# Optimization experiments

Hardware: AMD Instinct MI355X
Metric: run time of the kernel (lower is better)

Reference implementation:

```python
import jax, jax.numpy as jnp
import numpy as np

B, C, N = 4, 256, 4096
QK = 32  # query/key channel dim hardcoded in module


def setup_inputs() -> dict:
    key = jax.random.key(0)
    ks = jax.random.split(key, 5)
    sc = 1.0 / np.sqrt(C)
    return {
        "x": jax.random.normal(ks[0], (B, C, N), dtype=jnp.float32),
        "Wf": jax.random.normal(ks[1], (QK, C), dtype=jnp.float32) * sc,
        "bf": jnp.zeros((QK,), dtype=jnp.float32),
        "Wg": jax.random.normal(ks[2], (QK, C), dtype=jnp.float32) * sc,
        "bg": jnp.zeros((QK,), dtype=jnp.float32),
        "Wh": jax.random.normal(ks[3], (C, C), dtype=jnp.float32) * sc,
        "bh": jnp.zeros((C,), dtype=jnp.float32),
        "gamma": jax.random.normal(ks[4], (1,), dtype=jnp.float32) * 0.1,
    }


def reference(x, Wf, bf, Wg, bg, Wh, bh, gamma):
    # 1x1 Conv1d == channel-mixing matmul: (O,C) x (B,C,N) -> (B,O,N)
    f = jnp.einsum('oc,bcn->bon', Wf, x) + bf[:, None]   # (B, 32, N)
    g = jnp.einsum('oc,bcn->bon', Wg, x) + bg[:, None]   # (B, 32, N)
    h = jnp.einsum('oc,bcn->bon', Wh, x) + bh[:, None]   # (B, C, N)
    # attention[b, n, m] = sum_k f[b,k,n] * g[b,k,m]  (unscaled, per source)
    attn = jax.nn.softmax(jnp.einsum('bkn,bkm->bnm', f, g), axis=-1)  # (B,N,N)
    # torch.bmm(h, attention): out[b,c,m] = sum_n h[b,c,n] * attn[b,n,m]
    sa = jnp.einsum('bcn,bnm->bcm', h, attn)             # (B, C, N)
    return gamma * sa + x
```

## Files before the change

### kernel.cpp

```cpp
#include <hip/hip_runtime.h>
#include <hip/hip_bf16.h>
#include <math.h>

constexpr int Bb = 4;
constexpr int Cc = 256;
constexpr int Nn = 4096;
constexpr int K  = 32;

constexpr float LOG2E = 1.4426950408889634f;
constexpr float C40L  = 40.0f * LOG2E;

typedef __attribute__((ext_vector_type(8))) short short8;
typedef __attribute__((ext_vector_type(4))) float f32x4;
typedef __attribute__((ext_vector_type(2))) unsigned int uint2v;

static __device__ __forceinline__ unsigned int pack2(float a, float b) {
  union { __hip_bfloat162 h2; unsigned int u; } cv;
  cv.h2 = __float22bfloat162_rn(float2{a, b});
  return cv.u;
}
static __device__ __forceinline__ unsigned short f2bf(float f) {
  union { __hip_bfloat16 h; unsigned short u; } cv;
  cv.h = __float2bfloat16(f);
  return cv.u;
}
static __device__ __forceinline__ f32x4 MF(short8 a, short8 b, f32x4 c) {
  return __builtin_amdgcn_mfma_f32_16x16x32_bf16(a, b, c, 0, 0, 0);
}
static __device__ __forceinline__ float ex2(float v) {
  return __builtin_amdgcn_exp2f(v);
}
static __device__ __forceinline__ void stage16(const unsigned short* g,
                                               unsigned short* l) {
  __builtin_amdgcn_global_load_lds(
      (const __attribute__((address_space(1))) unsigned int*)g,
      (__attribute__((address_space(3))) unsigned int*)l, 16, 0, 0);
}


__global__ __launch_bounds__(256) void castW(
    const float* __restrict__ Wh, unsigned short* __restrict__ Whb)
{
  int i = (blockIdx.x * 256 + threadIdx.x) * 4;
  float4 v = *(const float4*)&Wh[i];
  uint2 o = { pack2(v.x, v.y), pack2(v.z, v.w) };
  *(uint2*)&Whb[i] = o;
}

__global__ __launch_bounds__(256) void castFG(
    const float* __restrict__ Wf, const float* __restrict__ Wg,
    unsigned short* __restrict__ Wfgb)
{
  int g = (blockIdx.x * 256 + threadIdx.x) * 4;
  int row = g >> 8, c = g & 255;
  const float* src = (row < 32) ? &Wf[row*Cc + c] : &Wg[(row-32)*Cc + c];
  float4 v = *(const float4*)src;
  uint2 o = { pack2(v.x, v.y), pack2(v.z, v.w) };
  *(uint2*)&Wfgb[g] = o;
}

__global__ __launch_bounds__(256) void trans_k(
    const float* __restrict__ x, unsigned short* __restrict__ xT)
{
  __shared__ unsigned short Ls[64][65];
  const int b  = blockIdx.z;
  const int n0 = blockIdx.x * 64, c0 = blockIdx.y * 64;
  const int tid = threadIdx.x;
  {
    const int cr = tid >> 4, n4 = (tid & 15) * 4;
#pragma unroll
    for (int rr = 0; rr < 4; ++rr) {
      int c = rr * 16 + cr;
      float4 v = *(const float4*)&x[(size_t)(b*Cc + c0 + c)*Nn + n0 + n4];
      Ls[c][n4+0] = f2bf(v.x); Ls[c][n4+1] = f2bf(v.y);
      Ls[c][n4+2] = f2bf(v.z); Ls[c][n4+3] = f2bf(v.w);
    }
  }
  __syncthreads();
  {
    const int nw = tid >> 4, cw = (tid & 15) * 4;
#pragma unroll
    for (int rr = 0; rr < 4; ++rr) {
      int n = nw + rr * 16;
      unsigned int lo = (unsigned int)Ls[cw+0][n] | ((unsigned int)Ls[cw+1][n] << 16);
      unsigned int hi = (unsigned int)Ls[cw+2][n] | ((unsigned int)Ls[cw+3][n] << 16);
      uint2 o = { lo, hi };
      *(uint2*)&xT[(size_t)(b*Nn + n0 + n)*Cc + c0 + cw] = o;
    }
  }
}

__global__ __launch_bounds__(256) void proj_fgM(
    const unsigned short* __restrict__ xT, const unsigned short* __restrict__ Wfgb,
    const float* __restrict__ bf, const float* __restrict__ bg,
    unsigned short* __restrict__ Ft, unsigned short* __restrict__ Gt)
{
  const int b = blockIdx.y;
  const int tid = threadIdx.x, wave = tid >> 6, lane = tid & 63;
  const int q = lane >> 4, col = lane & 15;
  const int n = blockIdx.x * 64 + wave * 16 + col;

  const unsigned short* Bp = xT + (size_t)(b*Nn + n)*Cc + q*8;
  const f32x4 zero = {0.f,0.f,0.f,0.f};
  f32x4 af0 = zero, af1 = zero, ag0 = zero, ag1 = zero;
#pragma unroll
  for (int kc = 0; kc < 8; ++kc) {
    short8 bn = *(const short8*)(Bp + kc*32);
    short8 a0 = *(const short8*)(Wfgb + (size_t)( 0 + col)*Cc + kc*32 + q*8);
    short8 a1 = *(const short8*)(Wfgb + (size_t)(16 + col)*Cc + kc*32 + q*8);
    short8 a2 = *(const short8*)(Wfgb + (size_t)(32 + col)*Cc + kc*32 + q*8);
    short8 a3 = *(const short8*)(Wfgb + (size_t)(48 + col)*Cc + kc*32 + q*8);
    af0 = MF(a0, bn, af0); af1 = MF(a1, bn, af1);
    ag0 = MF(a2, bn, ag0); ag1 = MF(a3, bn, ag1);
  }
  float4 bf0 = *(const float4*)&bf[q*4],      bf1 = *(const float4*)&bf[16 + q*4];
  float4 bg0 = *(const float4*)&bg[q*4],      bg1 = *(const float4*)&bg[16 + q*4];
  uint2 F0 = { pack2((af0[0]+bf0.x)*LOG2E, (af0[1]+bf0.y)*LOG2E),
               pack2((af0[2]+bf0.z)*LOG2E, (af0[3]+bf0.w)*LOG2E) };
  uint2 F1 = { pack2((af1[0]+bf1.x)*LOG2E, (af1[1]+bf1.y)*LOG2E),
               pack2((af1[2]+bf1.z)*LOG2E, (af1[3]+bf1.w)*LOG2E) };
  uint2 G0 = { pack2(ag0[0]+bg0.x, ag0[1]+bg0.y), pack2(ag0[2]+bg0.z, ag0[3]+bg0.w) };
  uint2 G1 = { pack2(ag1[0]+bg1.x, ag1[1]+bg1.y), pack2(ag1[2]+bg1.z, ag1[3]+bg1.w) };
  unsigned short* fo = Ft + (size_t)(b*Nn + n)*K;
  unsigned short* go = Gt + (size_t)(b*Nn + n)*K;
  *(uint2*)(fo + q*4) = F0;  *(uint2*)(fo + 16 + q*4) = F1;
  *(uint2*)(go + q*4) = G0;  *(uint2*)(go + 16 + q*4) = G1;
}

__global__ __launch_bounds__(512) void pass1(
    const unsigned short* __restrict__ Ft, const unsigned short* __restrict__ Gt,
    unsigned short* __restrict__ Et, float* __restrict__ Lp)
{
  __shared__ float red[8][64];
  const int n0 = blockIdx.x * 64;
  const int mh = blockIdx.y;
  const int b  = blockIdx.z;
  const int tid = threadIdx.x, wave = tid >> 6, lane = tid & 63;
  const int q = lane >> 4, col = lane & 15;
  const unsigned short* Fb = Ft + (size_t)b*Nn*K;
  const unsigned short* Gb = Gt + (size_t)b*Nn*K;
  unsigned short* Ebt = Et + (size_t)b*Nn*Nn;

  short8 af[4];
#pragma unroll
  for (int rb = 0; rb < 4; ++rb)
    af[rb] = *(const short8*)(Fb + (size_t)(n0 + rb*16 + col)*K + q*8);

  const int mw = mh*2048 + wave*256;
  const f32x4 cinit = {-C40L, -C40L, -C40L, -C40L};
  float l[16];
#pragma unroll
  for (int i = 0; i < 16; ++i) l[i] = 0.f;

  unsigned short* sbase = Ebt + (size_t)(n0 >> 3)*128
                        + (q >> 1)*128 + col*8 + (q & 1)*4;

  short8 gA = *(const short8*)(Gb + (size_t)(mw + col)*K + q*8);
  for (int it = 0; it < 16; ++it) {
    short8 gB = *(const short8*)(Gb + (size_t)(mw + ((it+1)&15)*16 + col)*K + q*8);
    f32x4 ts[4];
    ts[0] = MF(af[0], gA, cinit);
    ts[1] = MF(af[1], gA, cinit);
    ts[2] = MF(af[2], gA, cinit);
    ts[3] = MF(af[3], gA, cinit);
    const int mt = (mw >> 4) + it;
    unsigned short* sb = sbase + (size_t)mt * (Nn*16);
#pragma unroll
    for (int rb = 0; rb < 4; ++rb) {
      float e0 = ex2(ts[rb][0]), e1 = ex2(ts[rb][1]);
      float e2 = ex2(ts[rb][2]), e3 = ex2(ts[rb][3]);
      l[rb*4+0] += e0; l[rb*4+1] += e1; l[rb*4+2] += e2; l[rb*4+3] += e3;
      uint2v w = { pack2(e0, e1), pack2(e2, e3) };
      __builtin_nontemporal_store(w, (uint2v*)(sb + rb*256));
    }
    gA = gB;
  }
#pragma unroll
  for (int d = 1; d < 16; d <<= 1) {
#pragma unroll
    for (int i = 0; i < 16; ++i) l[i] += __shfl_xor(l[i], d);
  }
  if (col == 0) {
#pragma unroll
    for (int rb = 0; rb < 4; ++rb) {
      float4 v = {l[rb*4+0], l[rb*4+1], l[rb*4+2], l[rb*4+3]};
      *(float4*)&red[wave][rb*16 + q*4] = v;
    }
  }
  __syncthreads();
  if (tid < 64) {
    float t = 0.f;
#pragma unroll
    for (int w = 0; w < 8; ++w) t += red[w][tid];
    Lp[((size_t)mh*Bb + b)*Nn + n0 + tid] = t;
  }
}

__global__ __launch_bounds__(256) void sumL(
    const float* __restrict__ Lp, float* __restrict__ L)
{
  int i = blockIdx.x * 256 + threadIdx.x;
  L[i] = Lp[i] + Lp[(size_t)Bb*Nn + i];
}

__global__ __launch_bounds__(256) void proj_hT(
    const unsigned short* __restrict__ xT, const unsigned short* __restrict__ Whb,
    const float* __restrict__ bh, const float* __restrict__ L,
    const float* __restrict__ gamma, unsigned short* __restrict__ Ht)
{
  const int b   = blockIdx.z;
  const int n0  = blockIdx.x * 64;
  const int c0  = blockIdx.y * 64;
  const int tid = threadIdx.x;
  const int wave = tid >> 6, lane = tid & 63;
  const int q = lane >> 4, col = lane & 15;
  const int nw = n0 + wave * 16;

  const unsigned short* Arow  = xT  + (size_t)(b*Nn + nw + col) * Cc + q*8;
  const unsigned short* Bbase = Whb + (size_t)(c0 + col) * Cc + q*8;

  const f32x4 zero = {0.f,0.f,0.f,0.f};
  f32x4 acc[4] = {zero, zero, zero, zero};

  short8 a0 = *(const short8*)(Arow);
  short8 b0[4], b1[4];
#pragma unroll
  for (int j = 0; j < 4; ++j) b0[j] = *(const short8*)(Bbase + (size_t)(j*16)*Cc);

  for (int ks = 0; ks < 256; ks += 64) {
    int k1 = (ks + 32) & 255;
    short8 a1 = *(const short8*)(Arow + k1);
#pragma unroll
    for (int j = 0; j < 4; ++j) b1[j] = *(const short8*)(Bbase + (size_t)(j*16)*Cc + k1);
#pragma unroll
    for (int j = 0; j < 4; ++j) acc[j] = MF(a0, b0[j], acc[j]);
    int k2 = (ks + 64) & 255;
    a0 = *(const short8*)(Arow + k2);
#pragma unroll
    for (int j = 0; j < 4; ++j) b0[j] = *(const short8*)(Bbase + (size_t)(j*16)*Cc + k2);
#pragma unroll
    for (int j = 0; j < 4; ++j) acc[j] = MF(a1, b1[j], acc[j]);
  }

  const float gm = gamma[0];
  float4 lv = *(const float4*)&L[(size_t)b*Nn + nw + q*4];
  float linv[4] = {gm/lv.x, gm/lv.y, gm/lv.z, gm/lv.w};
  unsigned short* Hbt = Ht + (size_t)b*Cc*Nn;
  unsigned short* wb = Hbt + (size_t)(nw >> 3)*128 + (q >> 1)*128 + col*8 + (q & 1)*4;
#pragma unroll
  for (int j = 0; j < 4; ++j) {
    float bb = bh[c0 + j*16 + col];
    float v0 = (acc[j][0] + bb) * linv[0];
    float v1 = (acc[j][1] + bb) * linv[1];
    float v2 = (acc[j][2] + bb) * linv[2];
    float v3 = (acc[j][3] + bb) * linv[3];
    uint2v w = { pack2(v0, v1), pack2(v2, v3) };
    *(uint2v*)(wb + (size_t)((c0 >> 4) + j) * (Nn*16)) = w;
  }
}

__global__ __launch_bounds__(256) void initX(
    const float* __restrict__ x, float* __restrict__ out)
{
  size_t i = ((size_t)blockIdx.x * 256 + threadIdx.x) * 4;
  float4 v = *(const float4*)&x[i];
  *(float4*)&out[i] = v;
}

__global__ __launch_bounds__(256, 4) void out_gemm3(
    const unsigned short* __restrict__ Ht, const unsigned short* __restrict__ Et,
    float* __restrict__ out)
{
  __shared__ unsigned short As[2][4096];
  __shared__ unsigned short Bs[2][4096];
  constexpr int TS = Nn * 16;

  const int id = blockIdx.x;
  const int ct = id >> 9;
  const int r  = id & 511;
  const int mt = r >> 4;
  const int b  = (r >> 2) & 3;
  const int ks = r & 3;
  const int c0 = ct * 128;
  const int m0 = mt * 128;
  const int nb16 = ks * 16384;

  const int tid = threadIdx.x, wave = tid >> 6, lane = tid & 63;
  const int q = lane >> 4, col = lane & 15;
  const int wc = wave & 1, wm = wave >> 1;

  const unsigned short* Ag = Ht + (size_t)b*Cc*Nn + (size_t)(c0 >> 4)*TS + nb16;
  const unsigned short* Bg = Et + (size_t)b*Nn*Nn + (size_t)(m0 >> 4)*TS + nb16;

  auto stage = [&](int buf, int t) {
    const int kb = t * 512;
    if (wave < 2) {
      unsigned short* ld = &As[buf][0];
#pragma unroll
      for (int i = 0; i < 4; ++i) {
        int ct8 = wave*4 + i;
        stage16(Ag + (size_t)ct8*TS + kb + lane*8, ld + ct8*512);
      }
    } else {
      unsigned short* ld = &Bs[buf][0];
#pragma unroll
      for (int i = 0; i < 4; ++i) {
        int mt8 = (wave-2)*4 + i;
        stage16(Bg + (size_t)mt8*TS + kb + lane*8, ld + mt8*512);
      }
    }
  };

  const f32x4 zero = {0.f,0.f,0.f,0.f};
  f32x4 acc[4][4];
#pragma unroll
  for (int i = 0; i < 4; ++i)
#pragma unroll
    for (int j = 0; j < 4; ++j) acc[i][j] = zero;

  auto compute = [&](int buf) {
    short8 af[4], ef[4];
#pragma unroll
    for (int i = 0; i < 4; ++i) {
      af[i] = *(const short8*)&As[buf][(wc*4+i)*512 + q*128 + col*8];
      ef[i] = *(const short8*)&Bs[buf][(wm*4+i)*512 + q*128 + col*8];
    }
#pragma unroll
    for (int ci = 0; ci < 4; ++ci)
#pragma unroll
      for (int mi = 0; mi < 4; ++mi)
        acc[ci][mi] = MF(af[ci], ef[mi], acc[ci][mi]);
  };

  stage(0, 0);
  __syncthreads();
  for (int t = 0; t < 31; ++t) {
    stage((t + 1) & 1, t + 1);
    compute(t & 1);
    __syncthreads();
  }
  compute(1);

#pragma unroll
  for (int ci = 0; ci < 4; ++ci) {
#pragma unroll
    for (int mi = 0; mi < 4; ++mi) {
      const int m = m0 + wm*64 + mi*16 + col;
#pragma unroll
      for (int rr = 0; rr < 4; ++rr) {
        int c = c0 + wc*64 + ci*16 + q*4 + rr;
        atomicAdd(&out[((size_t)(b*Cc + c))*Nn + m], acc[ci][mi][rr]);
      }
    }
  }
}

__global__ __launch_bounds__(256) void proj_h(
    const unsigned short* __restrict__ xT, const unsigned short* __restrict__ Whb,
    const float* __restrict__ bh, unsigned short* __restrict__ H)
{
  const int b   = blockIdx.z;
  const int n0  = blockIdx.x * 64;
  const int c0  = blockIdx.y * 64;
  const int tid = threadIdx.x;
  const int wave = tid >> 6, lane = tid & 63;
  const int q = lane >> 4, col = lane & 15;
  const int cw = c0 + wave * 16;

  const unsigned short* Arow = Whb + (size_t)(cw + col) * Cc + q*8;
  const unsigned short* Bbase = xT + (size_t)(b*Nn + n0 + col) * Cc + q*8;

  const f32x4 zero = {0.f,0.f,0.f,0.f};
  f32x4 acc[4] = {zero, zero, zero, zero};

  short8 a0 = *(const short8*)(Arow);
  short8 b0[4], b1[4];
#pragma unroll
  for (int j = 0; j < 4; ++j) b0[j] = *(const short8*)(Bbase + (size_t)(j*16)*Cc);

  for (int ks = 0; ks < 256; ks += 64) {
    int k1 = (ks + 32) & 255;
    short8 a1 = *(const short8*)(Arow + k1);
#pragma unroll
    for (int j = 0; j < 4; ++j) b1[j] = *(const short8*)(Bbase + (size_t)(j*16)*Cc + k1);
#pragma unroll
    for (int j = 0; j < 4; ++j) acc[j] = MF(a0, b0[j], acc[j]);
    int k2 = (ks + 64) & 255;
    a0 = *(const short8*)(Arow + k2);
#pragma unroll
    for (int j = 0; j < 4; ++j) b0[j] = *(const short8*)(Bbase + (size_t)(j*16)*Cc + k2);
#pragma unroll
    for (int j = 0; j < 4; ++j) acc[j] = MF(a1, b1[j], acc[j]);
  }

  float4 bb = *(const float4*)&bh[cw + q*4];
  float brs[4] = {bb.x, bb.y, bb.z, bb.w};
#pragma unroll
  for (int j = 0; j < 4; ++j) {
#pragma unroll
    for (int r = 0; r < 4; ++r) {
      int c = cw + q*4 + r;
      int n = n0 + j*16 + col;
      H[(size_t)(b*Cc + c)*Nn + n] = f2bf(acc[j][r] + brs[r]);
    }
  }
}

__global__ __launch_bounds__(256) void stats_k(
    const unsigned short* __restrict__ Ft, const unsigned short* __restrict__ Gt,
    float* __restrict__ Lp)
{
  __shared__ float red[4][32];
  const int b = blockIdx.y >> 1, ms = blockIdx.y & 1;
  const int n0 = blockIdx.x * 32;
  const int tid = threadIdx.x, wave = tid >> 6, lane = tid & 63;
  const int q = lane >> 4, col = lane & 15;
  const unsigned short* Fb = Ft + (size_t)b*Nn*K;
  const unsigned short* Gb = Gt + (size_t)b*Nn*K;

  short8 af0 = *(const short8*)(Fb + (size_t)(n0      + col)*K + q*8);
  short8 af1 = *(const short8*)(Fb + (size_t)(n0 + 16 + col)*K + q*8);
  const int mq = ms*2048 + wave*512;
  const f32x4 zero = {0.f,0.f,0.f,0.f};
  float l[8] = {0.f,0.f,0.f,0.f,0.f,0.f,0.f,0.f};

  short8 gfA = *(const short8*)(Gb + (size_t)(mq + col)*K + q*8);
  for (int it = 0; it < 32; ++it) {
    short8 gfB = *(const short8*)(Gb + (size_t)(mq + ((it+1)&31)*16 + col)*K + q*8);
    f32x4 s0 = MF(af0, gfA, zero);
    f32x4 s1 = MF(af1, gfA, zero);
#pragma unroll
    for (int r = 0; r < 4; ++r) {
      l[r]   += ex2(s0[r] - C40L);
      l[4+r] += ex2(s1[r] - C40L);
    }
    gfA = gfB;
  }
#pragma unroll
  for (int d = 1; d < 16; d <<= 1) {
#pragma unroll
    for (int r = 0; r < 8; ++r) l[r] += __shfl_xor(l[r], d);
  }
  if (col == 0) {
    float4 v0 = {l[0], l[1], l[2], l[3]};
    float4 v1 = {l[4], l[5], l[6], l[7]};
    *(float4*)&red[wave][q*4]      = v0;
    *(float4*)&red[wave][16 + q*4] = v1;
  }
  __syncthreads();
  if (tid < 32) {
    float t = red[0][tid] + red[1][tid] + red[2][tid] + red[3][tid];
    Lp[((size_t)ms*Bb + b)*Nn + n0 + tid] = t;
  }
}

__global__ __launch_bounds__(256) void zcomb(
    const float* __restrict__ Lp, float* __restrict__ Z2)
{
  int i = blockIdx.x * 256 + threadIdx.x;
  Z2[i] = C40L + __log2f(Lp[i] + Lp[(size_t)Bb*Nn + i]);
}

struct Gen { short8 af0, af1; short8 hf[4]; };

__global__ __launch_bounds__(256, 4) void out_k(
    const unsigned short* __restrict__ Ft, const unsigned short* __restrict__ Gt,
    const unsigned short* __restrict__ H, const float* __restrict__ Z2,
    const float* __restrict__ x, const float* __restrict__ gamma,
    float* __restrict__ dst)
{
  __shared__ unsigned short Ps[4][32*40];
  const int b   = blockIdx.y;
  const int m0  = blockIdx.x * 64;
  const int c0b = blockIdx.z * 128;
  const int tid = threadIdx.x, wave = tid >> 6, lane = tid & 63;
  const int q = lane >> 4, col = lane & 15;
  const int mw  = m0 + (wave & 1) * 32;
  const int c0w = c0b + (wave >> 1) * 64;

  const unsigned short* Fb = Ft + (size_t)b*Nn*K;
  const unsigned short* Hb = H  + (size_t)b*Cc*Nn;
  const float*          Zb = Z2 + (size_t)b*Nn;

  short8 gf0 = *(const short8*)(Gt + (size_t)(b*Nn + mw      + col)*K + q*8);
  short8 gf1 = *(const short8*)(Gt + (size_t)(b*Nn + mw + 16 + col)*K + q*8);

  unsigned short* Pw = &Ps[wave][0];
  const f32x4 zero = {0.f,0.f,0.f,0.f};
  f32x4 acc[2][4];
#pragma unroll
  for (int j = 0; j < 2; ++j)
#pragma unroll
    for (int i = 0; i < 4; ++i) acc[j][i] = zero;

  Gen A, B;
  auto loadGen = [&](Gen& G, int nt) {
    G.af0 = *(const short8*)(Fb + (size_t)(nt      + col)*K + q*8);
    G.af1 = *(const short8*)(Fb + (size_t)(nt + 16 + col)*K + q*8);
#pragma unroll
    for (int i = 0; i < 4; ++i)
      G.hf[i] = *(const short8*)(Hb + (size_t)(c0w + i*16 + col)*Nn + nt + q*8);
  };
  auto step = [&](int nt, Gen& CUR, Gen& NXT) {
    loadGen(NXT, (nt + 32) & (Nn - 1));
    float4 z0 = *(const float4*)(Zb + nt + q*4);
    float4 z1 = *(const float4*)(Zb + nt + 16 + q*4);
    f32x4 s00 = MF(CUR.af0, gf0, zero);
    f32x4 s01 = MF(CUR.af0, gf1, zero);
    f32x4 s10 = MF(CUR.af1, gf0, zero);
    f32x4 s11 = MF(CUR.af1, gf1, zero);
    uint2 w00 = { pack2(ex2(s00[0]-z0.x), ex2(s00[1]-z0.y)),
                  pack2(ex2(s00[2]-z0.z), ex2(s00[3]-z0.w)) };
    uint2 w01 = { pack2(ex2(s01[0]-z0.x), ex2(s01[1]-z0.y)),
                  pack2(ex2(s01[2]-z0.z), ex2(s01[3]-z0.w)) };
    uint2 w10 = { pack2(ex2(s10[0]-z1.x), ex2(s10[1]-z1.y)),
                  pack2(ex2(s10[2]-z1.z), ex2(s10[3]-z1.w)) };
    uint2 w11 = { pack2(ex2(s11[0]-z1.x), ex2(s11[1]-z1.y)),
                  pack2(ex2(s11[2]-z1.z), ex2(s11[3]-z1.w)) };
    *(uint2*)&Pw[(     col)*40      + q*4] = w00;
    *(uint2*)&Pw[(16 + col)*40      + q*4] = w01;
    *(uint2*)&Pw[(     col)*40 + 16 + q*4] = w10;
    *(uint2*)&Pw[(16 + col)*40 + 16 + q*4] = w11;
    short8 pf0 = *(const short8*)&Pw[(     col)*40 + q*8];
    short8 pf1 = *(const short8*)&Pw[(16 + col)*40 + q*8];
#pragma unroll
    for (int i = 0; i < 4; ++i) {
      acc[0][i] = MF(CUR.hf[i], pf0, acc[0][i]);
      acc[1][i] = MF(CUR.hf[i], pf1, acc[1][i]);
    }
  };

  loadGen(A, 0);
  for (int t = 0; t < 128; t += 2) {
    step(t*32,      A, B);
    step(t*32 + 32, B, A);
  }

  const float gm = gamma[0];
#pragma unroll
  for (int mj = 0; mj < 2; ++mj) {
    const int m = mw + mj*16 + col;
#pragma unroll
    for (int i = 0; i < 4; ++i) {
#pragma unroll
      for (int r = 0; r < 4; ++r) {
        int c = c0w + i*16 + q*4 + r;
        size_t idx = ((size_t)(b*Cc + c))*Nn + m;
        dst[idx] = fmaf(gm, acc[mj][i][r], x[idx]);
      }
    }
  }
}

extern "C" void kernel_launch(void* const* d_in, const int* in_sizes, int n_in,
                              void* d_out, int out_size, void* d_ws, size_t ws_size,
                              hipStream_t stream) {
  (void)in_sizes; (void)n_in; (void)out_size;
  const float* x     = (const float*)d_in[0];
  const float* Wf    = (const float*)d_in[1];
  const float* bf    = (const float*)d_in[2];
  const float* Wg    = (const float*)d_in[3];
  const float* bg    = (const float*)d_in[4];
  const float* Wh    = (const float*)d_in[5];
  const float* bh    = (const float*)d_in[6];
  const float* gamma = (const float*)d_in[7];
  float* out = (float*)d_out;

  unsigned short* Ft   = (unsigned short*)d_ws;
  unsigned short* Gt   = Ft   + (size_t)Bb*Nn*K;
  unsigned short* xT   = Gt   + (size_t)Bb*Nn*K;
  unsigned short* H    = xT   + (size_t)Bb*Nn*Cc;
  unsigned short* Whb  = H    + (size_t)Bb*Cc*Nn;
  unsigned short* Wfgb = Whb  + (size_t)Cc*Cc;
  float*          L    = (float*)(Wfgb + 64*Cc);
  float*          Z2   = L  + (size_t)Bb*Nn;
  float*          Lp   = Z2 + (size_t)Bb*Nn;
  unsigned short* Et   = (unsigned short*)(Lp + 2*(size_t)Bb*Nn);

  const size_t baseEnd = 19038208ull + 65536ull*4;
  const size_t needE   = baseEnd + (size_t)Bb*Nn*Nn*2;

  castW   <<<dim3(Cc*Cc/1024), 256, 0, stream>>>(Wh, Whb);
  castFG  <<<dim3(64*Cc/1024), 256, 0, stream>>>(Wf, Wg, Wfgb);
  trans_k <<<dim3(Nn/64, Cc/64, Bb), 256, 0, stream>>>(x, xT);
  proj_fgM<<<dim3(Nn/64, Bb), 256, 0, stream>>>(xT, Wfgb, bf, bg, Ft, Gt);

  if (ws_size >= needE) {
    pass1    <<<dim3(Nn/64, 2, Bb), 512, 0, stream>>>(Ft, Gt, Et, Lp);
    sumL     <<<dim3(Bb*Nn/256), 256, 0, stream>>>(Lp, L);
    proj_hT  <<<dim3(Nn/64, Cc/64, Bb), 256, 0, stream>>>(xT, Whb, bh, L, gamma, H);
    initX    <<<dim3((size_t)Bb*Cc*Nn/1024), 256, 0, stream>>>(x, out);
    out_gemm3<<<dim3(1024), 256, 0, stream>>>(H, Et, out);
  } else {
    proj_h  <<<dim3(Nn/64, Cc/64, Bb), 256, 0, stream>>>(xT, Whb, bh, H);
    stats_k <<<dim3(Nn/32, 2*Bb), 256, 0, stream>>>(Ft, Gt, Lp);
    zcomb   <<<dim3(Bb*Nn/256), 256, 0, stream>>>(Lp, Z2);
    out_k   <<<dim3(Nn/64, Bb, 2), 256, 0, stream>>>(Ft, Gt, H, Z2, x, gamma, out);
  }
}
```

Baseline: 235.1 us.

## Fuse output init into transpose and deepen out-GEMM K tile with XCD-aware mapping

The copy of x into the output moves into the transpose kernel, which already reads x, so the separate initX launch and its extra read of x go away. The output GEMM now uses a K tile twice as deep per stage with double-sized shared buffers. It splits K two ways instead of four, which halves the grid to 512 blocks and halves the atomic or partial accumulation traffic into out. Block ids are remapped so each batch and K-split pair lands on one XCD, aiming for better L2 reuse, but occupancy drops to 2 blocks per CU.

Measured after the change: 210.2 us. 1.12x faster.

```diff
diff --git a/kernel.cpp b/kernel.cpp
--- a/kernel.cpp
+++ b/kernel.cpp
@@ -60,7 +60,8 @@
 }
 
 __global__ __launch_bounds__(256) void trans_k(
-    const float* __restrict__ x, unsigned short* __restrict__ xT)
+    const float* __restrict__ x, unsigned short* __restrict__ xT,
+    float* __restrict__ outInit)
 {
   __shared__ unsigned short Ls[64][65];
   const int b  = blockIdx.z;
@@ -71,7 +72,9 @@
 #pragma unroll
     for (int rr = 0; rr < 4; ++rr) {
       int c = rr * 16 + cr;
-      float4 v = *(const float4*)&x[(size_t)(b*Cc + c0 + c)*Nn + n0 + n4];
+      size_t idx = (size_t)(b*Cc + c0 + c)*Nn + n0 + n4;
+      float4 v = *(const float4*)&x[idx];
+      *(float4*)&outInit[idx] = v;
       Ls[c][n4+0] = f2bf(v.x); Ls[c][n4+1] = f2bf(v.y);
       Ls[c][n4+2] = f2bf(v.z); Ls[c][n4+3] = f2bf(v.w);
     }
@@ -259,31 +262,24 @@
   }
 }
 
-__global__ __launch_bounds__(256) void initX(
-    const float* __restrict__ x, float* __restrict__ out)
-{
-  size_t i = ((size_t)blockIdx.x * 256 + threadIdx.x) * 4;
-  float4 v = *(const float4*)&x[i];
-  *(float4*)&out[i] = v;
-}
-
-__global__ __launch_bounds__(256, 4) void out_gemm3(
+__global__ __launch_bounds__(256, 2) void out_gemm4(
     const unsigned short* __restrict__ Ht, const unsigned short* __restrict__ Et,
     float* __restrict__ out)
 {
-  __shared__ unsigned short As[2][4096];
-  __shared__ unsigned short Bs[2][4096];
+  __shared__ unsigned short As[2][8192];
+  __shared__ unsigned short Bs[2][8192];
   constexpr int TS = Nn * 16;
 
-  const int id = blockIdx.x;
-  const int ct = id >> 9;
-  const int r  = id & 511;
-  const int mt = r >> 4;
-  const int b  = (r >> 2) & 3;
-  const int ks = r & 3;
+  const int id  = blockIdx.x;
+  const int xcd = id & 7;
+  const int b   = xcd >> 1;
+  const int ks  = xcd & 1;
+  const int s   = id >> 3;
+  const int ct  = s >> 5;
+  const int mt  = s & 31;
   const int c0 = ct * 128;
   const int m0 = mt * 128;
-  const int nb16 = ks * 16384;
+  const int nb16 = ks * 32768;
 
   const int tid = threadIdx.x, wave = tid >> 6, lane = tid & 63;
   const int q = lane >> 4, col = lane & 15;
@@ -293,20 +289,22 @@
   const unsigned short* Bg = Et + (size_t)b*Nn*Nn + (size_t)(m0 >> 4)*TS + nb16;
 
   auto stage = [&](int buf, int t) {
-    const int kb = t * 512;
+    const int kb = t * 1024;
     if (wave < 2) {
       unsigned short* ld = &As[buf][0];
 #pragma unroll
-      for (int i = 0; i < 4; ++i) {
-        int ct8 = wave*4 + i;
-        stage16(Ag + (size_t)ct8*TS + kb + lane*8, ld + ct8*512);
+      for (int i = 0; i < 8; ++i) {
+        int j = wave*8 + i, ct8 = j >> 1, h2 = j & 1;
+        stage16(Ag + (size_t)ct8*TS + kb + h2*512 + lane*8,
+                ld + ct8*1024 + h2*512);
       }
     } else {
       unsigned short* ld = &Bs[buf][0];
 #pragma unroll
-      for (int i = 0; i < 4; ++i) {
-        int mt8 = (wave-2)*4 + i;
-        stage16(Bg + (size_t)mt8*TS + kb + lane*8, ld + mt8*512);
+      for (int i = 0; i < 8; ++i) {
+        int j = (wave-2)*8 + i, mt8 = j >> 1, h2 = j & 1;
+        stage16(Bg + (size_t)mt8*TS + kb + h2*512 + lane*8,
+                ld + mt8*1024 + h2*512);
       }
     }
   };
@@ -319,17 +317,20 @@
     for (int j = 0; j < 4; ++j) acc[i][j] = zero;
 
   auto compute = [&](int buf) {
-    short8 af[4], ef[4];
-#pragma unroll
-    for (int i = 0; i < 4; ++i) {
-      af[i] = *(const short8*)&As[buf][(wc*4+i)*512 + q*128 + col*8];
-      ef[i] = *(const short8*)&Bs[buf][(wm*4+i)*512 + q*128 + col*8];
-    }
-#pragma unroll
-    for (int ci = 0; ci < 4; ++ci)
-#pragma unroll
-      for (int mi = 0; mi < 4; ++mi)
-        acc[ci][mi] = MF(af[ci], ef[mi], acc[ci][mi]);
+#pragma unroll
+    for (int kc = 0; kc < 2; ++kc) {
+      short8 af[4], ef[4];
+#pragma unroll
+      for (int i = 0; i < 4; ++i) {
+        af[i] = *(const short8*)&As[buf][(wc*4+i)*1024 + (kc*4+q)*128 + col*8];
+        ef[i] = *(const short8*)&Bs[buf][(wm*4+i)*1024 + (kc*4+q)*128 + col*8];
+      }
+#pragma unroll
+      for (int ci = 0; ci < 4; ++ci)
+#pragma unroll
+        for (int mi = 0; mi < 4; ++mi)
+          acc[ci][mi] = MF(af[ci], ef[mi], acc[ci][mi]);
+    }
   };
 
   stage(0, 0);
@@ -582,15 +583,14 @@
 
   castW   <<<dim3(Cc*Cc/1024), 256, 0, stream>>>(Wh, Whb);
   castFG  <<<dim3(64*Cc/1024), 256, 0, stream>>>(Wf, Wg, Wfgb);
-  trans_k <<<dim3(Nn/64, Cc/64, Bb), 256, 0, stream>>>(x, xT);
+  trans_k <<<dim3(Nn/64, Cc/64, Bb), 256, 0, stream>>>(x, xT, out);
   proj_fgM<<<dim3(Nn/64, Bb), 256, 0, stream>>>(xT, Wfgb, bf, bg, Ft, Gt);
 
   if (ws_size >= needE) {
     pass1    <<<dim3(Nn/64, 2, Bb), 512, 0, stream>>>(Ft, Gt, Et, Lp);
     sumL     <<<dim3(Bb*Nn/256), 256, 0, stream>>>(Lp, L);
     proj_hT  <<<dim3(Nn/64, Cc/64, Bb), 256, 0, stream>>>(xT, Whb, bh, L, gamma, H);
-    initX    <<<dim3((size_t)Bb*Cc*Nn/1024), 256, 0, stream>>>(x, out);
-    out_gemm3<<<dim3(1024), 256, 0, stream>>>(H, Et, out);
+    out_gemm4<<<dim3(512), 256, 0, stream>>>(H, Et, out);
   } else {
     proj_h  <<<dim3(Nn/64, Cc/64, Bb), 256, 0, stream>>>(xT, Whb, bh, H);
     stats_k <<<dim3(Nn/32, 2*Bb), 256, 0, stream>>>(Ft, Gt, Lp);
```
